# Optimization experiments

Measured on AMD Instinct MI355X. Metric: run time of the kernel, lower is better.

The kernel has to match this reference:

```python
import jax, jax.numpy as jnp
import numpy as np


def setup_inputs() -> dict:
    key = jax.random.key(0)
    k1, k2 = jax.random.split(key)
    H = W = 2048
    valid = jnp.ones((H, W), dtype=bool)  # all pixels valid (index_map >= 0)
    candidates = jax.random.normal(k1, (H * W, 3), dtype=jnp.float32)
    candidates_norms = jax.random.normal(k2, (H * W, 3), dtype=jnp.float32)
    return {"valid": valid, "candidates": candidates,
            "candidates_norms": candidates_norms, "step": 2}


def _graph_outputs(valid, candidates, candidates_norms, step):
    # Grid-mesh graph build (init_graph) with all-valid map, expressed with
    # static shapes: invalid (out-of-grid) edges/faces are masked, not pruned.
    H, W = valid.shape
    us = jnp.arange(0, W - 1, step)
    vs = jnp.arange(0, H - 1, step)
    nu, nv = us.shape[0], vs.shape[0]
    N = nu * nv  # number of ED nodes (anchors)
    jj, ii = jnp.meshgrid(jnp.arange(nv), jnp.arange(nu), indexing='ij')
    jj = jj.ravel(); ii = ii.ravel()
    node = jj * nu + ii                      # node id == arange(N)
    pix = vs[jj] * W + us[ii]                # flattened pixel index of anchor
    pts = candidates[pix]                    # [N,3] ED node positions
    nrm = candidates_norms[pix]              # [N,3] ED node normals

    re = ii + 1 < nu                         # right neighbor exists
    de = jj + 1 < nv                         # down neighbor exists
    rd = re & de
    # 4-edge stencil per anchor: right, diag, down, anti-diag (matches init_graph)
    src = jnp.concatenate([node, node, node, node + 1])
    dst = jnp.concatenate([node + 1, node + nu + 1, node + nu, node + nu])
    emask = jnp.concatenate([re, rd, de, rd])          # [4N]
    srcs = jnp.where(emask, src, 0)
    dsts = jnp.where(emask, dst, 0)
    diff = pts[srcs] - pts[dsts]
    sq = jnp.sum(diff * diff, axis=1)
    w = emask.astype(pts.dtype)
    lens = jnp.sqrt(jnp.where(emask, sq, 1.0)) * w     # masked edge lengths

    # radii[k] = mean length of edges incident to node k (scatter-mean replaces
    # the original O(N) Python loop over torch.any(edge_index == k))
    ssum = (jax.ops.segment_sum(lens, srcs, num_segments=N)
            + jax.ops.segment_sum(lens, dsts, num_segments=N))
    cnt = (jax.ops.segment_sum(w, srcs, num_segments=N)
           + jax.ops.segment_sum(w, dsts, num_segments=N))
    radii = ssum / jnp.maximum(cnt, 1.0)
    has = cnt > 0
    mean_r = jnp.sum(jnp.where(has, radii, 0.0)) / jnp.maximum(
        jnp.sum(has.astype(pts.dtype)), 1.0)
    radii = jnp.where(has, radii, mean_r)  # NaN fix: fill isolated nodes w/ mean

    # two triangles per grid cell: (a, right, diag) and (a, diag, down)
    t0 = jnp.concatenate([node, node])
    t1 = jnp.concatenate([node + 1, node + nu + 1])
    t2 = jnp.concatenate([node + nu + 1, node + nu])
    tmask = jnp.concatenate([rd, rd])
    t0s = jnp.where(tmask, t0, 0)
    t1s = jnp.where(tmask, t1, 0)
    t2s = jnp.where(tmask, t2, 0)
    cr = jnp.cross(pts[t1s] - pts[t0s], pts[t2s] - pts[t0s], axis=1)
    areas = 0.5 * jnp.sqrt(jnp.sum(cr * cr, axis=1) + 1e-13)
    areas = areas * tmask.astype(pts.dtype)
    return pts, nrm, radii, lens, areas


def reference(valid, candidates, candidates_norms, step):
    return _graph_outputs(valid, candidates, candidates_norms, step)
```

## Files before the change

### kernel.cpp

```cpp
#include <hip/hip_runtime.h>
#include <math.h>


#define BX 64
#define BY 4
#define NC 131
#define RS (NC * 3)
#define RSP 400
#define NF4 100

struct F3 { float x, y, z; };

__device__ inline F3 ldl(const float* p, int o) {
    F3 r; r.x = p[o]; r.y = p[o + 1]; r.z = p[o + 2]; return r;
}

__device__ inline float dist3(const F3& a, const F3& b) {
    float dx = a.x - b.x, dy = a.y - b.y, dz = a.z - b.z;
    return sqrtf(dx * dx + dy * dy + dz * dz);
}

__global__ __launch_bounds__(256) void ddg_kernel(
    const float* __restrict__ cand, const float* __restrict__ cnorm,
    float* __restrict__ out, int W, int nu, int nv)
{
    __shared__ float sC[6 * RSP];
    __shared__ float sN[4 * RSP];

    const int H = W;
    const int tx = threadIdx.x, ty = threadIdx.y;
    const int tid = ty * BX + tx;
    const int i0 = blockIdx.x * BX;
    const int j0 = blockIdx.y * BY;
    const long c0 = 2L * i0 - 2;

    const float4* __restrict__ cand4  = (const float4*)cand;
    const float4* __restrict__ cnorm4 = (const float4*)cnorm;

    for (int idx = tid; idx < 10 * NF4; idx += BX * BY) {
        const int k = idx / NF4;
        const int t = idx - k * NF4;
        const bool isC = k < 6;
        int r = isC ? (2 * j0 - 2 + 2 * k) : (2 * (j0 + (k - 6)));
        r = min(max(r, 0), H - 2);
        const long f0 = ((long)r * W + c0) * 3;
        const long a0 = (f0 < 0 ? 0L : f0) & ~3L;
        const long q  = (a0 >> 2) + t;
        const float4 v = isC ? cand4[q] : cnorm4[q];
        const long G = q << 2;
        const long l = G - f0;
        float* dst = isC ? (sC + k * RSP) : (sN + (k - 6) * RSP);
        const float vv[4] = {v.x, v.y, v.z, v.w};
        #pragma unroll
        for (int c = 0; c < 4; ++c) {
            const long lc = l + c;
            if (lc >= 0 && lc < RS) dst[lc] = vv[c];
        }
    }
    __syncthreads();

    const int ii = i0 + tx, jj = j0 + ty;
    if (ii >= nu || jj >= nv) return;
    const int N = nu * nv;
    const int n = jj * nu + ii;
    const bool hr = (ii + 1) < nu, hd = (jj + 1) < nv;
    const bool hl = ii > 0,        hu = jj > 0;

    const float* rU = sC + ty * RSP;
    const float* rM = sC + (ty + 1) * RSP;
    const float* rD = sC + (ty + 2) * RSP;
    const int lL = (2 * tx) * 3;
    const int lM = (2 * tx + 2) * 3;
    const int lR = (2 * tx + 4) * 3;

    const F3 p00 = ldl(rM, lM);
    const F3 pr  = ldl(rM, lR);
    const F3 pl  = ldl(rM, lL);
    const F3 pu  = ldl(rU, lM);
    const F3 pd  = ldl(rD, lM);
    const F3 prd = ldl(rD, lR);
    const F3 pld = ldl(rD, lL);
    const F3 plu = ldl(rU, lL);
    const F3 pru = ldl(rU, lR);
    const F3 n00 = ldl(sN + ty * RSP, lM);

    const float len_r  = hr         ? dist3(p00, pr)  : 0.f;
    const float len_dg = (hr && hd) ? dist3(p00, prd) : 0.f;
    const float len_dn = hd         ? dist3(p00, pd)  : 0.f;
    const float len_ad = (hr && hd) ? dist3(pr, pd)   : 0.f;

    float a0f = 0.f, a1f = 0.f;
    if (hr && hd) {
        const float e1x = pr.x - p00.x,  e1y = pr.y - p00.y,  e1z = pr.z - p00.z;
        const float e2x = prd.x - p00.x, e2y = prd.y - p00.y, e2z = prd.z - p00.z;
        const float cx = e1y * e2z - e1z * e2y;
        const float cy = e1z * e2x - e1x * e2z;
        const float cz = e1x * e2y - e1y * e2x;
        a0f = 0.5f * sqrtf(cx * cx + cy * cy + cz * cz + 1e-13f);
        const float f2x = pd.x - p00.x, f2y = pd.y - p00.y, f2z = pd.z - p00.z;
        const float gx = e2y * f2z - e2z * f2y;
        const float gy = e2z * f2x - e2x * f2z;
        const float gz = e2x * f2y - e2y * f2x;
        a1f = 0.5f * sqrtf(gx * gx + gy * gy + gz * gz + 1e-13f);
    }

    float s = 0.f, cnt = 0.f;
    if (hr)       { s += len_r;           cnt += 1.f; }
    if (hr && hd) { s += len_dg;          cnt += 1.f; }
    if (hd)       { s += len_dn;          cnt += 1.f; }
    if (hl && hd) { s += dist3(p00, pld); cnt += 1.f; }
    if (hl)       { s += dist3(p00, pl);  cnt += 1.f; }
    if (hl && hu) { s += dist3(p00, plu); cnt += 1.f; }
    if (hu)       { s += dist3(p00, pu);  cnt += 1.f; }
    if (hr && hu) { s += dist3(p00, pru); cnt += 1.f; }
    const float radius = s / fmaxf(cnt, 1.f);

    float* __restrict__ pts   = out;
    float* __restrict__ nrm   = out + 3L * N;
    float* __restrict__ rad   = out + 6L * N;
    float* __restrict__ lens  = out + 7L * N;
    float* __restrict__ areas = out + 11L * N;

    pts[3L * n]     = p00.x; pts[3L * n + 1] = p00.y; pts[3L * n + 2] = p00.z;
    nrm[3L * n]     = n00.x; nrm[3L * n + 1] = n00.y; nrm[3L * n + 2] = n00.z;
    rad[n]          = radius;
    lens[n]             = len_r;
    lens[(long)N + n]   = len_dg;
    lens[2L * N + n]    = len_dn;
    lens[3L * N + n]    = len_ad;
    areas[n]            = a0f;
    areas[(long)N + n]  = a1f;
}

extern "C" void kernel_launch(void* const* d_in, const int* in_sizes, int n_in,
                              void* d_out, int out_size, void* d_ws, size_t ws_size,
                              hipStream_t stream) {
    const float* cand  = (const float*)d_in[1];
    const float* cnorm = (const float*)d_in[2];
    const int step = 2;
    const int HW = in_sizes[0];
    const int W = (int)(sqrt((double)HW) + 0.5);
    const int nu = (W - 1 + step - 1) / step;
    const int nv = nu;
    dim3 block(BX, BY);
    dim3 grid((nu + BX - 1) / BX, (nv + BY - 1) / BY);
    ddg_kernel<<<grid, block, 0, stream>>>(cand, cnorm, (float*)d_out, W, nu, nv);
}
```

Baseline: 147.3 us.

## Enlarge tile rows, simplify aligned float4 staging, load normals directly from global

Doubles block height to 8 rows (512 threads), so the 2-row halo is a smaller share of the candidate rows staged in shared memory. The staging loop now writes whole float4s at a fixed offset of -2 floats with no per-element bounds checks, and row pointers are shifted by 2 to compensate. Normals are no longer staged in shared memory and are read directly from global memory per thread as strided scalar loads. The uncoalesced normal reads and the larger block could lower occupancy, and the float4 read at the last column relies on rows being contiguous.

```diff
diff --git a/kernel.cpp b/kernel.cpp
--- a/kernel.cpp
+++ b/kernel.cpp
@@ -3,11 +3,12 @@
 
 
 #define BX 64
-#define BY 4
-#define NC 131
+#define BY 8
+#define NROWS (BY + 2)
+#define NC (2 * BX + 3)
 #define RS (NC * 3)
 #define RSP 400
-#define NF4 100
+#define NF4 99
 
 struct F3 { float x, y, z; };
 
@@ -20,12 +21,12 @@
     return sqrtf(dx * dx + dy * dy + dz * dz);
 }
 
-__global__ __launch_bounds__(256) void ddg_kernel(
+__global__ __launch_bounds__(512) void ddg_kernel(
     const float* __restrict__ cand, const float* __restrict__ cnorm,
     float* __restrict__ out, int W, int nu, int nv)
 {
-    __shared__ float sC[6 * RSP];
-    __shared__ float sN[4 * RSP];
+    __shared__ float4 sC4[NROWS * (RSP / 4)];
+    float* const sC = (float*)sC4;
 
     const int H = W;
     const int tx = threadIdx.x, ty = threadIdx.y;
@@ -34,28 +35,16 @@
     const int j0 = blockIdx.y * BY;
     const long c0 = 2L * i0 - 2;
 
-    const float4* __restrict__ cand4  = (const float4*)cand;
-    const float4* __restrict__ cnorm4 = (const float4*)cnorm;
-
-    for (int idx = tid; idx < 10 * NF4; idx += BX * BY) {
+    const float4* __restrict__ cand4 = (const float4*)cand;
+    for (int idx = tid; idx < NROWS * NF4; idx += BX * BY) {
         const int k = idx / NF4;
         const int t = idx - k * NF4;
-        const bool isC = k < 6;
-        int r = isC ? (2 * j0 - 2 + 2 * k) : (2 * (j0 + (k - 6)));
+        int r = 2 * j0 - 2 + 2 * k;
         r = min(max(r, 0), H - 2);
         const long f0 = ((long)r * W + c0) * 3;
-        const long a0 = (f0 < 0 ? 0L : f0) & ~3L;
-        const long q  = (a0 >> 2) + t;
-        const float4 v = isC ? cand4[q] : cnorm4[q];
-        const long G = q << 2;
-        const long l = G - f0;
-        float* dst = isC ? (sC + k * RSP) : (sN + (k - 6) * RSP);
-        const float vv[4] = {v.x, v.y, v.z, v.w};
-        #pragma unroll
-        for (int c = 0; c < 4; ++c) {
-            const long lc = l + c;
-            if (lc >= 0 && lc < RS) dst[lc] = vv[c];
-        }
+        long q = ((f0 - 2) >> 2) + t;
+        if (q < 0) q = 0;
+        ((float4*)(sC + k * RSP))[t] = cand4[q];
     }
     __syncthreads();
 
@@ -66,12 +55,12 @@
     const bool hr = (ii + 1) < nu, hd = (jj + 1) < nv;
     const bool hl = ii > 0,        hu = jj > 0;
 
-    const float* rU = sC + ty * RSP;
-    const float* rM = sC + (ty + 1) * RSP;
-    const float* rD = sC + (ty + 2) * RSP;
-    const int lL = (2 * tx) * 3;
-    const int lM = (2 * tx + 2) * 3;
-    const int lR = (2 * tx + 4) * 3;
+    const float* rU = sC + ty * RSP + 2;
+    const float* rM = sC + (ty + 1) * RSP + 2;
+    const float* rD = sC + (ty + 2) * RSP + 2;
+    const int lL = 6 * tx;
+    const int lM = lL + 6;
+    const int lR = lL + 12;
 
     const F3 p00 = ldl(rM, lM);
     const F3 pr  = ldl(rM, lR);
@@ -82,7 +71,9 @@
     const F3 pld = ldl(rD, lL);
     const F3 plu = ldl(rU, lL);
     const F3 pru = ldl(rU, lR);
-    const F3 n00 = ldl(sN + ty * RSP, lM);
+
+    const long pn = ((long)(2 * jj) * W + 2 * ii) * 3;
+    F3 n00; n00.x = cnorm[pn]; n00.y = cnorm[pn + 1]; n00.z = cnorm[pn + 2];
 
     const float len_r  = hr         ? dist3(p00, pr)  : 0.f;
     const float len_dg = (hr && hd) ? dist3(p00, prd) : 0.f;
```

Measured after the change: 143.6 us. -2.5%, faster.
